# Kernel optimization log

Measured on AMD Instinct MI355X. Metric: run time of the kernel, lower is better.

The kernel has to match this reference:

```python
import jax, jax.numpy as jnp
from jax import lax
import numpy as np

# FlowNetC correlation configuration (matches init_kwargs)
PAD = 20          # pad_size
K = 1             # kernel_size (kernel_radius = 0)
MAX_DISP = 20     # max_displacement
S1 = 1            # stride1
S2 = 2            # stride2
R = MAX_DISP // S2          # neighborhood_grid_radius = 10
GW = 2 * R + 1              # neighborhood_grid_width = 21
NOUT = GW * GW              # 441 output planes


def setup_inputs() -> dict:
    key = jax.random.key(0)
    k1, k2 = jax.random.split(key)
    B, C, H, W = 8, 256, 96, 128
    return {
        "input1": jax.random.normal(k1, (B, C, H, W), dtype=jnp.float32),
        "input2": jax.random.normal(k2, (B, C, H, W), dtype=jnp.float32),
    }


def _correlation(input1, input2):
    B, C, H, W = input1.shape
    # pad second input; with kernel_size=1 and pad==max_displacement the
    # output grid is exactly the input grid, and displaced pixel (y+dy, x+dx)
    # lives at padded index (y + PAD + dy, x + PAD + dx).
    p2 = jnp.pad(input2, ((0, 0), (0, 0), (PAD, PAD), (PAD, PAD)))
    sumelems = jnp.asarray(K * K * C, dtype=input1.dtype)

    def body(o):
        # displacement (dy, dx) = ((o//GW - R)*S2, (o%GW - R)*S2);
        # slice start in padded coords = PAD + d = (o//GW)*S2, (o%GW)*S2
        dy = (o // GW) * S2
        dx = (o % GW) * S2
        sl = lax.dynamic_slice(p2, (0, 0, dy, dx), (B, C, H, W))
        return jnp.einsum('bchw,bchw->bhw', input1, sl) / sumelems

    out = lax.map(body, jnp.arange(NOUT))       # [441, B, H, W]
    return jnp.transpose(out, (1, 0, 2, 3))     # [B, 441, H, W]


def reference(input1, input2):
    return _correlation(input1, input2)
```

## Files before the change

### kernel.cpp

```cpp
#include <hip/hip_runtime.h>
#include <hip/hip_bf16.h>


typedef __attribute__((ext_vector_type(8))) short bf16x8;
typedef __attribute__((ext_vector_type(4))) float f32x4;
typedef __attribute__((ext_vector_type(4))) unsigned u32x4;

constexpr int Bn = 8, Cn = 256, Hn = 96, Wn = 128, GW = 21;
constexpr int KC = 32, NCH = Cn / KC;
constexpr int NWG = Bn * Hn * GW;
constexpr int JW = 23;
constexpr size_t TELEMS = (size_t)Bn * Hn * NCH * 2048;

__device__ inline unsigned pack_bf16(float lo, float hi) {
    __hip_bfloat16 l = __float2bfloat16(lo);
    __hip_bfloat16 h = __float2bfloat16(hi);
    unsigned short lu, hu;
    __builtin_memcpy(&lu, &l, 2);
    __builtin_memcpy(&hu, &h, 2);
    return (unsigned)lu | ((unsigned)hu << 16);
}

__global__ __launch_bounds__(256) void prepack(
    const float* __restrict__ in1, const float* __restrict__ in2,
    unsigned* __restrict__ T)
{
    unsigned u = blockIdx.x;
    int ch = u & 7;  u >>= 3;
    int y  = u % 96; u /= 96;
    int b  = u & 7;  u >>= 3;
    const float* src = u ? in2 : in1;

    int t  = threadIdx.x;
    int tm = t & 63;
    int tg = t >> 6;

    const size_t chw = (size_t)Hn * Wn;
    const float* p = src + ((size_t)(b * Cn + ch * 32 + 8 * tg)) * chw
                         + (size_t)y * Wn + 2 * tm;
    float2 f[8];
#pragma unroll
    for (int k = 0; k < 8; ++k)
        f[k] = *(const float2*)(p + (size_t)k * chw);

    u32x4 ae, ao;
#pragma unroll
    for (int ku = 0; ku < 4; ++ku) {
        ae[ku] = pack_bf16(f[2 * ku].x, f[2 * ku + 1].x);
        ao[ku] = pack_bf16(f[2 * ku].y, f[2 * ku + 1].y);
    }
    unsigned* To = T + u * TELEMS + ((size_t)(b * Hn + y) * NCH + ch) * 2048
                     + ((tm >> 4) * 4 + tg) * 64 + (tm & 15) * 4;
    *(u32x4*)(To)        = ae;
    *(u32x4*)(To + 1024) = ao;
}

__global__ __launch_bounds__(256) void corr_frag(
    const unsigned* __restrict__ T1, const unsigned* __restrict__ T2,
    float* __restrict__ out)
{
    __shared__ float sout[Wn * JW];

    int orig = blockIdx.x;
    int xcd  = orig & 7;
    int i    = orig >> 3;
    int yw   = i % 3;  int t = i / 3;
    int dyi  = t % 21; t /= 21;
    int sub  = t & 1;
    int par  = (t >> 1) & 1;
    int b    = t >> 2;
    int y    = 12 * xcd + par + 2 * (3 * sub + yw);

    int y2  = y + 2 * dyi - 20;
    bool y2ok = (y2 >= 0) && (y2 < Hn);

    int tid = threadIdx.x;
    int w   = tid >> 6;
    int l   = tid & 63;
    int p   = w >> 1;
    int h   = w & 1;
    int g   = l >> 4;
    int m16 = l & 15;

    f32x4 acc[2][4] = {};

    if (y2ok) {
        const unsigned* pa = T1 + (size_t)(b * Hn + y)  * (NCH * 2048)
                                + p * 1024 + g * 64 + m16 * 4;
        const unsigned* pb = T2 + (size_t)(b * Hn + y2) * (NCH * 2048)
                                + p * 1024 + g * 64 + m16 * 4;

        bf16x8 ca0, ca1, cb0, cb1, cb2, cb3;
        ca0 = *(const bf16x8*)(pa + (2 * h + 0) * 256);
        ca1 = *(const bf16x8*)(pa + (2 * h + 1) * 256);
        cb0 = *(const bf16x8*)(pb + 0 * 256);
        cb1 = *(const bf16x8*)(pb + 1 * 256);
        cb2 = *(const bf16x8*)(pb + 2 * 256);
        cb3 = *(const bf16x8*)(pb + 3 * 256);

        for (int ch = 0; ch < NCH; ++ch) {
            bf16x8 na0, na1, nb0, nb1, nb2, nb3;
            if (ch + 1 < NCH) {
                const unsigned* A = pa + (ch + 1) * 2048;
                const unsigned* B = pb + (ch + 1) * 2048;
                na0 = *(const bf16x8*)(A + (2 * h + 0) * 256);
                na1 = *(const bf16x8*)(A + (2 * h + 1) * 256);
                nb0 = *(const bf16x8*)(B + 0 * 256);
                nb1 = *(const bf16x8*)(B + 1 * 256);
                nb2 = *(const bf16x8*)(B + 2 * 256);
                nb3 = *(const bf16x8*)(B + 3 * 256);
            }
            acc[0][0] = __builtin_amdgcn_mfma_f32_16x16x32_bf16(ca0, cb0, acc[0][0], 0, 0, 0);
            acc[0][1] = __builtin_amdgcn_mfma_f32_16x16x32_bf16(ca0, cb1, acc[0][1], 0, 0, 0);
            acc[0][2] = __builtin_amdgcn_mfma_f32_16x16x32_bf16(ca0, cb2, acc[0][2], 0, 0, 0);
            acc[0][3] = __builtin_amdgcn_mfma_f32_16x16x32_bf16(ca0, cb3, acc[0][3], 0, 0, 0);
            acc[1][0] = __builtin_amdgcn_mfma_f32_16x16x32_bf16(ca1, cb0, acc[1][0], 0, 0, 0);
            acc[1][1] = __builtin_amdgcn_mfma_f32_16x16x32_bf16(ca1, cb1, acc[1][1], 0, 0, 0);
            acc[1][2] = __builtin_amdgcn_mfma_f32_16x16x32_bf16(ca1, cb2, acc[1][2], 0, 0, 0);
            acc[1][3] = __builtin_amdgcn_mfma_f32_16x16x32_bf16(ca1, cb3, acc[1][3], 0, 0, 0);
            ca0 = na0; ca1 = na1;
            cb0 = nb0; cb1 = nb1; cb2 = nb2; cb3 = nb3;
        }
    }

    for (int i2 = tid; i2 < Wn * JW; i2 += 256) sout[i2] = 0.0f;
    __syncthreads();

    if (y2ok) {
        const float scale = 1.0f / 256.0f;
#pragma unroll
        for (int a = 0; a < 2; ++a)
#pragma unroll
            for (int n = 0; n < 4; ++n)
#pragma unroll
                for (int r = 0; r < 4; ++r) {
                    int xp = (2 * h + a) * 16 + g * 4 + r;
                    int up = n * 16 + m16;
                    int j  = up - xp + 10;
                    if ((unsigned)j < 21u)
                        sout[(2 * xp + p) * JW + j] = acc[a][n][r] * scale;
                }
    }
    __syncthreads();

    unsigned base0 = (unsigned)(((b * (GW * GW) + dyi * GW) * Hn + y) * Wn);
    constexpr unsigned PLANE = (unsigned)(Hn * Wn);
    for (int s = tid; s < GW * Wn; s += 256) {
        int j = s >> 7;
        int x = s & 127;
        out[base0 + (unsigned)j * PLANE + (unsigned)x] = sout[x * JW + j];
    }
}

__device__ inline void lds_barrier() {
    asm volatile("s_waitcnt lgkmcnt(0)" ::: "memory");
    __builtin_amdgcn_s_barrier();
    __builtin_amdgcn_sched_barrier(0);
}

__global__ __launch_bounds__(256) void corr_mfma_fb(
    const float* __restrict__ in1, const float* __restrict__ in2,
    float* __restrict__ out)
{
    __shared__ unsigned lds[4][1024];
    int orig = blockIdx.x;
    int xcd  = orig & 7;
    int i    = orig >> 3;
    int yw   = i % 3;  int t = i / 3;
    int dyi  = t % 21; t /= 21;
    int sub  = t & 1;
    int par  = (t >> 1) & 1;
    int b    = t >> 2;
    int y    = 12 * xcd + par + 2 * (3 * sub + yw);
    int y2  = y + 2 * dyi - 20;
    bool y2ok = (y2 >= 0) && (y2 < Hn);

    int tid = threadIdx.x;
    int w   = tid >> 6;
    int l   = tid & 63;
    int p   = w >> 1;
    int h   = w & 1;
    int g   = l >> 4;
    int m16 = l & 15;

    const size_t chw = (size_t)Hn * Wn;
    const float* pA = in1 + ((size_t)b * Cn) * chw + (size_t)y * Wn;
    const float* pB = in2 + ((size_t)b * Cn) * chw + (size_t)(y2ok ? y2 : 0) * Wn;

    int tm = tid & 63;
    int tg = tid >> 6;
    const int loff = ((tm >> 4) * 4 + tg) * 64 + (tm & 15) * 4;

    f32x4 acc[2][4] = {};
    float ax[8], ay[8], bx[8], by[8];

    auto prefetch = [&](int chunk) {
        size_t base = (size_t)(chunk * KC + 8 * tg) * chw + 2 * tm;
#pragma unroll
        for (int k = 0; k < 8; ++k) {
            float2 tA = *(const float2*)(pA + base + (size_t)k * chw);
            float2 tB = *(const float2*)(pB + base + (size_t)k * chw);
            ax[k] = tA.x; ay[k] = tA.y;
            bx[k] = tB.x; by[k] = tB.y;
        }
        __builtin_amdgcn_sched_barrier(0);
    };
    auto writeout = [&]() {
#pragma unroll
        for (int k = 0; k < 8; ++k)
            asm volatile("" : "+v"(ax[k]), "+v"(ay[k]), "+v"(bx[k]), "+v"(by[k]));
        u32x4 ae, ao, be, bo;
#pragma unroll
        for (int ku = 0; ku < 4; ++ku) {
            ae[ku] = pack_bf16(ax[2 * ku], ax[2 * ku + 1]);
            ao[ku] = pack_bf16(ay[2 * ku], ay[2 * ku + 1]);
            be[ku] = pack_bf16(bx[2 * ku], bx[2 * ku + 1]);
            bo[ku] = pack_bf16(by[2 * ku], by[2 * ku + 1]);
        }
        *(u32x4*)&lds[0][loff] = ae;
        *(u32x4*)&lds[1][loff] = ao;
        *(u32x4*)&lds[2][loff] = be;
        *(u32x4*)&lds[3][loff] = bo;
    };
    auto compute = [&]() {
        const unsigned* Pa = &lds[p][0];
        const unsigned* Pb = &lds[2 + p][0];
        int fo = g * 64 + m16 * 4;
        bf16x8 A0  = *(const bf16x8*)(Pa + (2 * h + 0) * 256 + fo);
        bf16x8 A1  = *(const bf16x8*)(Pa + (2 * h + 1) * 256 + fo);
        bf16x8 Bf0 = *(const bf16x8*)(Pb + 0 * 256 + fo);
        bf16x8 Bf1 = *(const bf16x8*)(Pb + 1 * 256 + fo);
        bf16x8 Bf2 = *(const bf16x8*)(Pb + 2 * 256 + fo);
        bf16x8 Bf3 = *(const bf16x8*)(Pb + 3 * 256 + fo);
        acc[0][0] = __builtin_amdgcn_mfma_f32_16x16x32_bf16(A0, Bf0, acc[0][0], 0, 0, 0);
        acc[0][1] = __builtin_amdgcn_mfma_f32_16x16x32_bf16(A0, Bf1, acc[0][1], 0, 0, 0);
        acc[0][2] = __builtin_amdgcn_mfma_f32_16x16x32_bf16(A0, Bf2, acc[0][2], 0, 0, 0);
        acc[0][3] = __builtin_amdgcn_mfma_f32_16x16x32_bf16(A0, Bf3, acc[0][3], 0, 0, 0);
        acc[1][0] = __builtin_amdgcn_mfma_f32_16x16x32_bf16(A1, Bf0, acc[1][0], 0, 0, 0);
        acc[1][1] = __builtin_amdgcn_mfma_f32_16x16x32_bf16(A1, Bf1, acc[1][1], 0, 0, 0);
        acc[1][2] = __builtin_amdgcn_mfma_f32_16x16x32_bf16(A1, Bf2, acc[1][2], 0, 0, 0);
        acc[1][3] = __builtin_amdgcn_mfma_f32_16x16x32_bf16(A1, Bf3, acc[1][3], 0, 0, 0);
    };

    if (y2ok) {
        prefetch(0);
        for (int it = 0; it < NCH; ++it) {
            writeout();
            lds_barrier();
            if (it + 1 < NCH) prefetch(it + 1);
            compute();
            lds_barrier();
        }
    }

    __syncthreads();
    float* sout = (float*)&lds[0][0];
    for (int i2 = tid; i2 < Wn * JW; i2 += 256) sout[i2] = 0.0f;
    __syncthreads();
    if (y2ok) {
        const float scale = 1.0f / 256.0f;
#pragma unroll
        for (int a = 0; a < 2; ++a)
#pragma unroll
            for (int n = 0; n < 4; ++n)
#pragma unroll
                for (int r = 0; r < 4; ++r) {
                    int xp = (2 * h + a) * 16 + g * 4 + r;
                    int up = n * 16 + m16;
                    int j  = up - xp + 10;
                    if ((unsigned)j < 21u)
                        sout[(2 * xp + p) * JW + j] = acc[a][n][r] * scale;
                }
    }
    __syncthreads();
    unsigned base0 = (unsigned)(((b * (GW * GW) + dyi * GW) * Hn + y) * Wn);
    constexpr unsigned PLANE = (unsigned)(Hn * Wn);
    for (int s = tid; s < GW * Wn; s += 256) {
        int j = s >> 7;
        int x = s & 127;
        out[base0 + (unsigned)j * PLANE + (unsigned)x] = sout[x * JW + j];
    }
}

extern "C" void kernel_launch(void* const* d_in, const int* in_sizes, int n_in,
                              void* d_out, int out_size, void* d_ws, size_t ws_size,
                              hipStream_t stream) {
    const float* in1 = (const float*)d_in[0];
    const float* in2 = (const float*)d_in[1];
    float* out = (float*)d_out;
    size_t need = 2 * TELEMS * sizeof(unsigned);
    if (ws_size >= need) {
        unsigned* T = (unsigned*)d_ws;
        prepack<<<2 * Bn * Hn * NCH, 256, 0, stream>>>(in1, in2, T);
        corr_frag<<<NWG, 256, 0, stream>>>(T, T + TELEMS, out);
    } else {
        corr_mfma_fb<<<NWG, 256, 0, stream>>>(in1, in2, out);
    }
}
```

Before: 186.7 us.

## Skip off-band MFMA tiles and split channel reduction across wave pairs

The correlation kernel now computes only the 10 of 16 16x16 MFMA tiles that intersect the 21-wide displacement band. Channel chunks are split between the two waves of each pair (h) instead of splitting the output rows, and the two partial sums are combined in shared memory at store time. This removes redundant matrix work for tiles whose results were discarded. In exchange it doubles the LDS buffer, adds an extra read and add per output, and drops the explicit next-chunk prefetch.

```diff
diff --git a/kernel.cpp b/kernel.cpp
--- a/kernel.cpp
+++ b/kernel.cpp
@@ -55,11 +55,11 @@
     *(u32x4*)(To + 1024) = ao;
 }
 
-__global__ __launch_bounds__(256) void corr_frag(
+__global__ __launch_bounds__(256) void corr_fragk(
     const unsigned* __restrict__ T1, const unsigned* __restrict__ T2,
     float* __restrict__ out)
 {
-    __shared__ float sout[Wn * JW];
+    __shared__ float sout[2][Wn * JW];
 
     int orig = blockIdx.x;
     int xcd  = orig & 7;
@@ -82,64 +82,55 @@
     int g   = l >> 4;
     int m16 = l & 15;
 
-    f32x4 acc[2][4] = {};
+    f32x4 acc[10] = {};
 
     if (y2ok) {
         const unsigned* pa = T1 + (size_t)(b * Hn + y)  * (NCH * 2048)
-                                + p * 1024 + g * 64 + m16 * 4;
+                                + p * 1024 + g * 64 + m16 * 4 + (size_t)h * 2048;
         const unsigned* pb = T2 + (size_t)(b * Hn + y2) * (NCH * 2048)
-                                + p * 1024 + g * 64 + m16 * 4;
-
-        bf16x8 ca0, ca1, cb0, cb1, cb2, cb3;
-        ca0 = *(const bf16x8*)(pa + (2 * h + 0) * 256);
-        ca1 = *(const bf16x8*)(pa + (2 * h + 1) * 256);
-        cb0 = *(const bf16x8*)(pb + 0 * 256);
-        cb1 = *(const bf16x8*)(pb + 1 * 256);
-        cb2 = *(const bf16x8*)(pb + 2 * 256);
-        cb3 = *(const bf16x8*)(pb + 3 * 256);
-
-        for (int ch = 0; ch < NCH; ++ch) {
-            bf16x8 na0, na1, nb0, nb1, nb2, nb3;
-            if (ch + 1 < NCH) {
-                const unsigned* A = pa + (ch + 1) * 2048;
-                const unsigned* B = pb + (ch + 1) * 2048;
-                na0 = *(const bf16x8*)(A + (2 * h + 0) * 256);
-                na1 = *(const bf16x8*)(A + (2 * h + 1) * 256);
-                nb0 = *(const bf16x8*)(B + 0 * 256);
-                nb1 = *(const bf16x8*)(B + 1 * 256);
-                nb2 = *(const bf16x8*)(B + 2 * 256);
-                nb3 = *(const bf16x8*)(B + 3 * 256);
+                                + p * 1024 + g * 64 + m16 * 4 + (size_t)h * 2048;
+
+        for (int ch = 0; ch < NCH / 2; ++ch) {
+            const unsigned* A = pa + (size_t)ch * 4096;
+            const unsigned* B = pb + (size_t)ch * 4096;
+            bf16x8 a0 = *(const bf16x8*)(A + 0 * 256);
+            bf16x8 a1 = *(const bf16x8*)(A + 1 * 256);
+            bf16x8 a2 = *(const bf16x8*)(A + 2 * 256);
+            bf16x8 a3 = *(const bf16x8*)(A + 3 * 256);
+            bf16x8 b0 = *(const bf16x8*)(B + 0 * 256);
+            bf16x8 b1 = *(const bf16x8*)(B + 1 * 256);
+            bf16x8 b2 = *(const bf16x8*)(B + 2 * 256);
+            bf16x8 b3 = *(const bf16x8*)(B + 3 * 256);
+            acc[0] = __builtin_amdgcn_mfma_f32_16x16x32_bf16(a0, b0, acc[0], 0, 0, 0);
+            acc[1] = __builtin_amdgcn_mfma_f32_16x16x32_bf16(a0, b1, acc[1], 0, 0, 0);
+            acc[2] = __builtin_amdgcn_mfma_f32_16x16x32_bf16(a1, b0, acc[2], 0, 0, 0);
+            acc[3] = __builtin_amdgcn_mfma_f32_16x16x32_bf16(a1, b1, acc[3], 0, 0, 0);
+            acc[4] = __builtin_amdgcn_mfma_f32_16x16x32_bf16(a1, b2, acc[4], 0, 0, 0);
+            acc[5] = __builtin_amdgcn_mfma_f32_16x16x32_bf16(a2, b1, acc[5], 0, 0, 0);
+            acc[6] = __builtin_amdgcn_mfma_f32_16x16x32_bf16(a2, b2, acc[6], 0, 0, 0);
+            acc[7] = __builtin_amdgcn_mfma_f32_16x16x32_bf16(a2, b3, acc[7], 0, 0, 0);
+            acc[8] = __builtin_amdgcn_mfma_f32_16x16x32_bf16(a3, b2, acc[8], 0, 0, 0);
+            acc[9] = __builtin_amdgcn_mfma_f32_16x16x32_bf16(a3, b3, acc[9], 0, 0, 0);
+        }
+    }
+
+    for (int i2 = tid; i2 < 2 * Wn * JW; i2 += 256) (&sout[0][0])[i2] = 0.0f;
+    __syncthreads();
+
+    if (y2ok) {
+        const float scale = 1.0f / 256.0f;
+        const int mtT[10] = {0,0,1,1,1,2,2,2,3,3};
+        const int ntT[10] = {0,1,0,1,2,1,2,3,2,3};
+#pragma unroll
+        for (int tt = 0; tt < 10; ++tt)
+#pragma unroll
+            for (int r = 0; r < 4; ++r) {
+                int xp = mtT[tt] * 16 + g * 4 + r;
+                int up = ntT[tt] * 16 + m16;
+                int j  = up - xp + 10;
+                if ((unsigned)j < 21u)
+                    sout[h][(2 * xp + p) * JW + j] = acc[tt][r] * scale;
             }
-            acc[0][0] = __builtin_amdgcn_mfma_f32_16x16x32_bf16(ca0, cb0, acc[0][0], 0, 0, 0);
-            acc[0][1] = __builtin_amdgcn_mfma_f32_16x16x32_bf16(ca0, cb1, acc[0][1], 0, 0, 0);
-            acc[0][2] = __builtin_amdgcn_mfma_f32_16x16x32_bf16(ca0, cb2, acc[0][2], 0, 0, 0);
-            acc[0][3] = __builtin_amdgcn_mfma_f32_16x16x32_bf16(ca0, cb3, acc[0][3], 0, 0, 0);
-            acc[1][0] = __builtin_amdgcn_mfma_f32_16x16x32_bf16(ca1, cb0, acc[1][0], 0, 0, 0);
-            acc[1][1] = __builtin_amdgcn_mfma_f32_16x16x32_bf16(ca1, cb1, acc[1][1], 0, 0, 0);
-            acc[1][2] = __builtin_amdgcn_mfma_f32_16x16x32_bf16(ca1, cb2, acc[1][2], 0, 0, 0);
-            acc[1][3] = __builtin_amdgcn_mfma_f32_16x16x32_bf16(ca1, cb3, acc[1][3], 0, 0, 0);
-            ca0 = na0; ca1 = na1;
-            cb0 = nb0; cb1 = nb1; cb2 = nb2; cb3 = nb3;
-        }
-    }
-
-    for (int i2 = tid; i2 < Wn * JW; i2 += 256) sout[i2] = 0.0f;
-    __syncthreads();
-
-    if (y2ok) {
-        const float scale = 1.0f / 256.0f;
-#pragma unroll
-        for (int a = 0; a < 2; ++a)
-#pragma unroll
-            for (int n = 0; n < 4; ++n)
-#pragma unroll
-                for (int r = 0; r < 4; ++r) {
-                    int xp = (2 * h + a) * 16 + g * 4 + r;
-                    int up = n * 16 + m16;
-                    int j  = up - xp + 10;
-                    if ((unsigned)j < 21u)
-                        sout[(2 * xp + p) * JW + j] = acc[a][n][r] * scale;
-                }
     }
     __syncthreads();
 
@@ -148,7 +139,8 @@
     for (int s = tid; s < GW * Wn; s += 256) {
         int j = s >> 7;
         int x = s & 127;
-        out[base0 + (unsigned)j * PLANE + (unsigned)x] = sout[x * JW + j];
+        out[base0 + (unsigned)j * PLANE + (unsigned)x] =
+            sout[0][x * JW + j] + sout[1][x * JW + j];
     }
 }
 
@@ -292,7 +284,7 @@
     if (ws_size >= need) {
         unsigned* T = (unsigned*)d_ws;
         prepack<<<2 * Bn * Hn * NCH, 256, 0, stream>>>(in1, in2, T);
-        corr_frag<<<NWG, 256, 0, stream>>>(T, T + TELEMS, out);
+        corr_fragk<<<NWG, 256, 0, stream>>>(T, T + TELEMS, out);
     } else {
         corr_mfma_fb<<<NWG, 256, 0, stream>>>(in1, in2, out);
     }
```

After: 178.2 us. 1.05x faster.

## Skip out-of-band MFMA tiles and deepen load prefetch to three stages

Applied to the files above, without the earlier changes.

Each wave now loads only the three B tiles that overlap its displacement band, offset by its half index, and issues five MFMAs per chunk instead of eight, skipping tiles whose outputs all fall outside the 21-wide band. The single-stage register prefetch becomes a fully unrolled triple-buffered pipeline with sched_barrier fences, so more global loads are in flight while MFMAs run. The cost is higher register pressure and a branch on h inside the compute step, and correctness depends on the skipped tiles truly producing no in-band outputs.

```diff
diff --git a/kernel.cpp b/kernel.cpp
--- a/kernel.cpp
+++ b/kernel.cpp
@@ -88,39 +88,49 @@
         const unsigned* pa = T1 + (size_t)(b * Hn + y)  * (NCH * 2048)
                                 + p * 1024 + g * 64 + m16 * 4;
         const unsigned* pb = T2 + (size_t)(b * Hn + y2) * (NCH * 2048)
-                                + p * 1024 + g * 64 + m16 * 4;
-
-        bf16x8 ca0, ca1, cb0, cb1, cb2, cb3;
-        ca0 = *(const bf16x8*)(pa + (2 * h + 0) * 256);
-        ca1 = *(const bf16x8*)(pa + (2 * h + 1) * 256);
-        cb0 = *(const bf16x8*)(pb + 0 * 256);
-        cb1 = *(const bf16x8*)(pb + 1 * 256);
-        cb2 = *(const bf16x8*)(pb + 2 * 256);
-        cb3 = *(const bf16x8*)(pb + 3 * 256);
-
-        for (int ch = 0; ch < NCH; ++ch) {
-            bf16x8 na0, na1, nb0, nb1, nb2, nb3;
-            if (ch + 1 < NCH) {
-                const unsigned* A = pa + (ch + 1) * 2048;
-                const unsigned* B = pb + (ch + 1) * 2048;
-                na0 = *(const bf16x8*)(A + (2 * h + 0) * 256);
-                na1 = *(const bf16x8*)(A + (2 * h + 1) * 256);
-                nb0 = *(const bf16x8*)(B + 0 * 256);
-                nb1 = *(const bf16x8*)(B + 1 * 256);
-                nb2 = *(const bf16x8*)(B + 2 * 256);
-                nb3 = *(const bf16x8*)(B + 3 * 256);
-            }
-            acc[0][0] = __builtin_amdgcn_mfma_f32_16x16x32_bf16(ca0, cb0, acc[0][0], 0, 0, 0);
-            acc[0][1] = __builtin_amdgcn_mfma_f32_16x16x32_bf16(ca0, cb1, acc[0][1], 0, 0, 0);
-            acc[0][2] = __builtin_amdgcn_mfma_f32_16x16x32_bf16(ca0, cb2, acc[0][2], 0, 0, 0);
-            acc[0][3] = __builtin_amdgcn_mfma_f32_16x16x32_bf16(ca0, cb3, acc[0][3], 0, 0, 0);
-            acc[1][0] = __builtin_amdgcn_mfma_f32_16x16x32_bf16(ca1, cb0, acc[1][0], 0, 0, 0);
-            acc[1][1] = __builtin_amdgcn_mfma_f32_16x16x32_bf16(ca1, cb1, acc[1][1], 0, 0, 0);
-            acc[1][2] = __builtin_amdgcn_mfma_f32_16x16x32_bf16(ca1, cb2, acc[1][2], 0, 0, 0);
-            acc[1][3] = __builtin_amdgcn_mfma_f32_16x16x32_bf16(ca1, cb3, acc[1][3], 0, 0, 0);
-            ca0 = na0; ca1 = na1;
-            cb0 = nb0; cb1 = nb1; cb2 = nb2; cb3 = nb3;
-        }
+                                + p * 1024 + g * 64 + m16 * 4 + h * 256;
+
+        bf16x8 A0[3], A1[3], B0[3], B1[3], B2[3];
+
+#define ISSUE(k) {                                                          \
+            const unsigned* A = pa + (k) * 2048;                            \
+            const unsigned* B = pb + (k) * 2048;                            \
+            A0[(k) % 3] = *(const bf16x8*)(A + (2 * h + 0) * 256);          \
+            A1[(k) % 3] = *(const bf16x8*)(A + (2 * h + 1) * 256);          \
+            B0[(k) % 3] = *(const bf16x8*)(B + 0 * 256);                    \
+            B1[(k) % 3] = *(const bf16x8*)(B + 1 * 256);                    \
+            B2[(k) % 3] = *(const bf16x8*)(B + 2 * 256);                    \
+        }
+#define COMPUTE(k) {                                                        \
+            __builtin_amdgcn_sched_barrier(0);                              \
+            bf16x8 a0 = A0[(k) % 3], a1 = A1[(k) % 3];                      \
+            bf16x8 b0 = B0[(k) % 3], b1 = B1[(k) % 3], b2 = B2[(k) % 3];    \
+            if (h == 0) {                                                   \
+                acc[0][0] = __builtin_amdgcn_mfma_f32_16x16x32_bf16(a0, b0, acc[0][0], 0, 0, 0); \
+                acc[0][1] = __builtin_amdgcn_mfma_f32_16x16x32_bf16(a0, b1, acc[0][1], 0, 0, 0); \
+                acc[1][0] = __builtin_amdgcn_mfma_f32_16x16x32_bf16(a1, b0, acc[1][0], 0, 0, 0); \
+                acc[1][1] = __builtin_amdgcn_mfma_f32_16x16x32_bf16(a1, b1, acc[1][1], 0, 0, 0); \
+                acc[1][2] = __builtin_amdgcn_mfma_f32_16x16x32_bf16(a1, b2, acc[1][2], 0, 0, 0); \
+            } else {                                                        \
+                acc[0][1] = __builtin_amdgcn_mfma_f32_16x16x32_bf16(a0, b0, acc[0][1], 0, 0, 0); \
+                acc[0][2] = __builtin_amdgcn_mfma_f32_16x16x32_bf16(a0, b1, acc[0][2], 0, 0, 0); \
+                acc[0][3] = __builtin_amdgcn_mfma_f32_16x16x32_bf16(a0, b2, acc[0][3], 0, 0, 0); \
+                acc[1][2] = __builtin_amdgcn_mfma_f32_16x16x32_bf16(a1, b1, acc[1][2], 0, 0, 0); \
+                acc[1][3] = __builtin_amdgcn_mfma_f32_16x16x32_bf16(a1, b2, acc[1][3], 0, 0, 0); \
+            }                                                               \
+        }
+
+        ISSUE(0); ISSUE(1); ISSUE(2);
+        COMPUTE(0); ISSUE(3);
+        COMPUTE(1); ISSUE(4);
+        COMPUTE(2); ISSUE(5);
+        COMPUTE(3); ISSUE(6);
+        COMPUTE(4); ISSUE(7);
+        COMPUTE(5);
+        COMPUTE(6);
+        COMPUTE(7);
+#undef ISSUE
+#undef COMPUTE
     }
 
     for (int i2 = tid; i2 < Wn * JW; i2 += 256) sout[i2] = 0.0f;
```

Measured after the change: 164.7 us. 1.13x faster.
